# Kernel tuning notes

Measured on AMD Instinct MI355X. Metric: run time of the kernel, lower is better.

Reference implementation:

```python
import jax, jax.numpy as jnp
import numpy as np

TOP_K = 2
CAP_FACTOR = 1.25
AUX_COEF = 0.01
Z_COEF = 0.001


def setup_inputs() -> dict:
    key = jax.random.key(0)
    k1, k2 = jax.random.split(key)
    hidden_states = jax.random.normal(k1, (4, 1024, 4096), dtype=jnp.float32)
    # gate_proj weight, torch Linear layout [out=E, in=H]
    W = jax.random.normal(k2, (8, 4096), dtype=jnp.float32) * 0.02
    return {"hidden_states": hidden_states, "W": W}


def reference(hidden_states, W):
    B, S, H = hidden_states.shape
    E = W.shape[0]
    T = B * S
    K = TOP_K
    C = max(int(T * K / E * CAP_FACTOR), 1)  # expert capacity

    x = hidden_states.reshape(T, H)
    gate_logits = x @ W.T                           # [T, E]
    top_v, top_i = jax.lax.top_k(gate_logits, K)    # [T, K]
    top_w = jax.nn.softmax(top_v, axis=-1)          # [T, K]

    # Flatten assignments in (token-major, k-minor) order, matching the
    # sequential python loop. Slot within an expert = number of prior
    # assignments to that expert (exclusive prefix count).
    e = top_i.reshape(-1)                           # [T*K]
    oh = jax.nn.one_hot(e, E, dtype=jnp.int32)      # [T*K, E]
    pos = jnp.sum(jnp.cumsum(oh, axis=0) * oh, axis=-1) - 1  # [T*K]
    valid = pos < C
    pos_c = jnp.minimum(pos, C - 1)
    tok = jnp.arange(T * K) // K
    w = top_w.reshape(-1)

    combine_weights = jnp.zeros((T, E, C), dtype=hidden_states.dtype)
    combine_weights = combine_weights.at[tok, e, pos_c].add(jnp.where(valid, w, 0.0))
    dispatch_mask = jnp.zeros((T, E, C), dtype=jnp.int32)
    dispatch_mask = dispatch_mask.at[tok, e, pos_c].add(valid.astype(jnp.int32)).astype(bool)

    # aux losses (module is in training mode by default)
    gate_probs = jax.nn.softmax(gate_logits, axis=-1)
    mean_gate_prob = gate_probs.mean(axis=0)                      # [E]
    tokens_per_expert = dispatch_mask.sum(axis=(0, 2)).astype(jnp.float32)
    tokens_per_expert = tokens_per_expert / tokens_per_expert.sum()
    load_balancing_loss = AUX_COEF * E * jnp.sum(mean_gate_prob * tokens_per_expert)
    router_z_loss = Z_COEF * jnp.mean(jax.nn.logsumexp(gate_logits, axis=-1))

    return dispatch_mask, combine_weights, top_i, load_balancing_loss, router_z_loss
```

## Files before the change

kernel.cpp:

```cpp
#include <hip/hip_runtime.h>
#include <math.h>

#define TT   4096
#define HH   4096
#define EE   8
#define KTOP 2
#define CAP  1280
#define TEC  ((size_t)TT * EE * CAP)

#define GATE_BLOCKS 256
#define ZERO_BLOCKS 4096

typedef __attribute__((ext_vector_type(4))) float f32x4;


__global__ __launch_bounds__(256) void fused_kernel(
    const float* __restrict__ x, const float* __restrict__ W,
    float* __restrict__ out, float* __restrict__ ws_part,
    int* __restrict__ ws_e, float* __restrict__ ws_w)
{
    int tid = threadIdx.x;

    if (blockIdx.x >= GATE_BLOCKS) {
        size_t zb = blockIdx.x - GATE_BLOCKS;
        f32x4* p = (f32x4*)out;
        const size_t per = (2 * TEC / 4) / ZERO_BLOCKS;
        size_t base = zb * per;
        f32x4 z = {0.f, 0.f, 0.f, 0.f};
#pragma unroll 4
        for (size_t i = tid; i < per; i += 256)
            __builtin_nontemporal_store(z, &p[base + i]);
        return;
    }

    __shared__ float bacc[9];
    if (tid < 9) bacc[tid] = 0.f;
    __syncthreads();

    int wave = tid >> 6;
    int lane = tid & 63;
    int t0 = (blockIdx.x * 4 + wave) * 4;

    const float4* __restrict__ W4 = (const float4*)W;
    const float4* __restrict__ X4 = (const float4*)x;

    float acc[4][8];
#pragma unroll
    for (int tt = 0; tt < 4; ++tt)
#pragma unroll
        for (int e = 0; e < 8; ++e) acc[tt][e] = 0.f;

    for (int jj = 0; jj < 16; ++jj) {
        int ci = jj * 64 + lane;
        float4 wv[8];
#pragma unroll
        for (int e = 0; e < 8; ++e) wv[e] = W4[e * 1024 + ci];
#pragma unroll
        for (int tt = 0; tt < 4; ++tt) {
            float4 xv = X4[(size_t)(t0 + tt) * 1024 + ci];
#pragma unroll
            for (int e = 0; e < 8; ++e) {
                acc[tt][e] = fmaf(xv.x, wv[e].x, acc[tt][e]);
                acc[tt][e] = fmaf(xv.y, wv[e].y, acc[tt][e]);
                acc[tt][e] = fmaf(xv.z, wv[e].z, acc[tt][e]);
                acc[tt][e] = fmaf(xv.w, wv[e].w, acc[tt][e]);
            }
        }
    }

#pragma unroll
    for (int tt = 0; tt < 4; ++tt)
#pragma unroll
        for (int e = 0; e < 8; ++e) {
#pragma unroll
            for (int s = 32; s >= 1; s >>= 1)
                acc[tt][e] += __shfl_xor(acc[tt][e], s, 64);
        }

    if (lane == 0) {
        for (int tt = 0; tt < 4; ++tt) {
            int t = t0 + tt;
            float l[8];
#pragma unroll
            for (int e = 0; e < 8; ++e) l[e] = acc[tt][e];

            float m = l[0];
#pragma unroll
            for (int e = 1; e < 8; ++e) m = fmaxf(m, l[e]);
            float p[8], s = 0.f;
#pragma unroll
            for (int e = 0; e < 8; ++e) { p[e] = expf(l[e] - m); s += p[e]; }
            float inv = 1.f / s;
#pragma unroll
            for (int e = 0; e < 8; ++e) atomicAdd(&bacc[e], p[e] * inv);
            atomicAdd(&bacc[8], m + logf(s));

            int i0 = 0;
#pragma unroll
            for (int e = 1; e < 8; ++e) if (l[e] > l[i0]) i0 = e;
            int i1 = (i0 == 0) ? 1 : 0;
#pragma unroll
            for (int e = 0; e < 8; ++e) if (e != i0 && l[e] > l[i1]) i1 = e;

            float w0 = 1.f / (1.f + expf(l[i1] - l[i0]));
            float w1 = 1.f - w0;

            float* out_topi = out + 2 * TEC;
            out_topi[t * 2 + 0] = (float)i0;
            out_topi[t * 2 + 1] = (float)i1;
            ws_e[t * 2 + 0] = i0;
            ws_e[t * 2 + 1] = i1;
            ws_w[t * 2 + 0] = w0;
            ws_w[t * 2 + 1] = w1;
        }
    }
    __syncthreads();
    if (tid < 9) ws_part[blockIdx.x * 9 + tid] = bacc[tid];
}

__global__ __launch_bounds__(256) void assign_kernel(
    const int* __restrict__ ws_e, const float* __restrict__ ws_w,
    const float* __restrict__ ws_part, float* __restrict__ out)
{
    __shared__ int   scnt[256][8];
    __shared__ int   ssum[8][8];
    __shared__ int   stot[8];
    __shared__ float lacc[9];

    int tid = threadIdx.x;
    if (tid < 9) lacc[tid] = 0.f;
    __syncthreads();

#pragma unroll
    for (int j = 0; j < 9; ++j)
        atomicAdd(&lacc[j], ws_part[tid * 9 + j]);

    const int PER = (TT * KTOP) / 256;
    int i0 = tid * PER;
    int cnt[8];
#pragma unroll
    for (int e = 0; e < 8; ++e) cnt[e] = 0;
    for (int j = 0; j < PER; ++j) cnt[ws_e[i0 + j]]++;
#pragma unroll
    for (int e = 0; e < 8; ++e) scnt[tid][e] = cnt[e];
    __syncthreads();

    if (tid < 64) {
        int e = tid & 7, seg = tid >> 3;
        int run = 0;
        for (int j = seg * 32; j < seg * 32 + 32; ++j) {
            int v = scnt[j][e];
            scnt[j][e] = run;
            run += v;
        }
        ssum[seg][e] = run;
    }
    __syncthreads();
    if (tid < 8) {
        int run = 0;
        for (int s = 0; s < 8; ++s) {
            int v = ssum[s][tid];
            ssum[s][tid] = run;
            run += v;
        }
        stot[tid] = run;
    }
    __syncthreads();

    int seg = tid >> 5;
    int base[8];
#pragma unroll
    for (int e = 0; e < 8; ++e) base[e] = scnt[tid][e] + ssum[seg][e];

    for (int j = 0; j < PER; ++j) {
        int i = i0 + j;
        int e = ws_e[i];
        int pos = base[e]++;
        if (pos < CAP) {
            int tok = i >> 1;
            size_t idx = (size_t)tok * (EE * CAP) + (size_t)e * CAP + pos;
            out[idx] = 1.0f;
            out[TEC + idx] = ws_w[i];
        }
    }
    __syncthreads();

    if (tid == 0) {
        int tot_valid = 0;
        int ve[8];
#pragma unroll
        for (int e = 0; e < 8; ++e) { ve[e] = min(stot[e], CAP); tot_valid += ve[e]; }
        float lbl = 0.f;
#pragma unroll
        for (int e = 0; e < 8; ++e)
            lbl += (lacc[e] / (float)TT) * ((float)ve[e] / (float)tot_valid);
        lbl *= 0.01f * (float)EE;
        float zl = 0.001f * lacc[8] / (float)TT;
        out[2 * TEC + TT * KTOP + 0] = lbl;
        out[2 * TEC + TT * KTOP + 1] = zl;
    }
}

extern "C" void kernel_launch(void* const* d_in, const int* in_sizes, int n_in,
                              void* d_out, int out_size, void* d_ws, size_t ws_size,
                              hipStream_t stream) {
    const float* x = (const float*)d_in[0];
    const float* W = (const float*)d_in[1];
    float* out = (float*)d_out;

    float* ws_part = (float*)d_ws;
    int*   ws_e    = (int*)((char*)d_ws + GATE_BLOCKS * 9 * 4);
    float* ws_w    = (float*)((char*)d_ws + GATE_BLOCKS * 9 * 4 + (size_t)TT * KTOP * 4);

    fused_kernel<<<GATE_BLOCKS + ZERO_BLOCKS, 256, 0, stream>>>(
        x, W, out, ws_part, ws_e, ws_w);

    assign_kernel<<<1, 256, 0, stream>>>(ws_e, ws_w, ws_part, out);
}
```

Before: 108.8 us.

## Split gate, scan, and zero-plus-scatter into three kernels with wider gate grid

The gate GEMV now uses 1024 blocks, with four waves splitting the hidden dimension of each 4-token group and combining partial sums through shared memory. Per-token softmax stats are written to the workspace and summed in the scan kernel. The scan kernel now only computes slot positions, and a new kernel zeroes each 2-token slab of the two big outputs and then scatters that slab's entries, removing the serial single-block scatter. The cost is an extra launch, the zero fill no longer overlapping the gate work, and regular stores replacing the nontemporal ones.

Result: slower. 113.1 us (+3.9%).

```diff
diff --git a/kernel.cpp b/kernel.cpp
--- a/kernel.cpp
+++ b/kernel.cpp
@@ -8,41 +8,26 @@
 #define CAP  1280
 #define TEC  ((size_t)TT * EE * CAP)
 
-#define GATE_BLOCKS 256
-#define ZERO_BLOCKS 4096
+#define GATE_BLOCKS 1024
+#define ZS_BLOCKS   4096
 
 typedef __attribute__((ext_vector_type(4))) float f32x4;
 
 
-__global__ __launch_bounds__(256) void fused_kernel(
+__global__ __launch_bounds__(256) void gate_kernel(
     const float* __restrict__ x, const float* __restrict__ W,
     float* __restrict__ out, float* __restrict__ ws_part,
     int* __restrict__ ws_e, float* __restrict__ ws_w)
 {
-    int tid = threadIdx.x;
-
-    if (blockIdx.x >= GATE_BLOCKS) {
-        size_t zb = blockIdx.x - GATE_BLOCKS;
-        f32x4* p = (f32x4*)out;
-        const size_t per = (2 * TEC / 4) / ZERO_BLOCKS;
-        size_t base = zb * per;
-        f32x4 z = {0.f, 0.f, 0.f, 0.f};
-#pragma unroll 4
-        for (size_t i = tid; i < per; i += 256)
-            __builtin_nontemporal_store(z, &p[base + i]);
-        return;
-    }
-
-    __shared__ float bacc[9];
-    if (tid < 9) bacc[tid] = 0.f;
-    __syncthreads();
-
+    __shared__ float wpart[4][4][8];
+
+    int tid  = threadIdx.x;
     int wave = tid >> 6;
     int lane = tid & 63;
-    int t0 = (blockIdx.x * 4 + wave) * 4;
-
+    int t0   = blockIdx.x * 4;
+
+    const float4* __restrict__ X4 = (const float4*)x;
     const float4* __restrict__ W4 = (const float4*)W;
-    const float4* __restrict__ X4 = (const float4*)x;
 
     float acc[4][8];
 #pragma unroll
@@ -50,8 +35,9 @@
 #pragma unroll
         for (int e = 0; e < 8; ++e) acc[tt][e] = 0.f;
 
-    for (int jj = 0; jj < 16; ++jj) {
-        int ci = jj * 64 + lane;
+#pragma unroll
+    for (int j = 0; j < 4; ++j) {
+        int ci = wave * 256 + j * 64 + lane;
         float4 wv[8];
 #pragma unroll
         for (int e = 0; e < 8; ++e) wv[e] = W4[e * 1024 + ci];
@@ -78,49 +64,55 @@
         }
 
     if (lane == 0) {
-        for (int tt = 0; tt < 4; ++tt) {
-            int t = t0 + tt;
-            float l[8];
-#pragma unroll
-            for (int e = 0; e < 8; ++e) l[e] = acc[tt][e];
-
-            float m = l[0];
-#pragma unroll
-            for (int e = 1; e < 8; ++e) m = fmaxf(m, l[e]);
-            float p[8], s = 0.f;
-#pragma unroll
-            for (int e = 0; e < 8; ++e) { p[e] = expf(l[e] - m); s += p[e]; }
-            float inv = 1.f / s;
-#pragma unroll
-            for (int e = 0; e < 8; ++e) atomicAdd(&bacc[e], p[e] * inv);
-            atomicAdd(&bacc[8], m + logf(s));
-
-            int i0 = 0;
-#pragma unroll
-            for (int e = 1; e < 8; ++e) if (l[e] > l[i0]) i0 = e;
-            int i1 = (i0 == 0) ? 1 : 0;
-#pragma unroll
-            for (int e = 0; e < 8; ++e) if (e != i0 && l[e] > l[i1]) i1 = e;
-
-            float w0 = 1.f / (1.f + expf(l[i1] - l[i0]));
-            float w1 = 1.f - w0;
-
-            float* out_topi = out + 2 * TEC;
-            out_topi[t * 2 + 0] = (float)i0;
-            out_topi[t * 2 + 1] = (float)i1;
-            ws_e[t * 2 + 0] = i0;
-            ws_e[t * 2 + 1] = i1;
-            ws_w[t * 2 + 0] = w0;
-            ws_w[t * 2 + 1] = w1;
-        }
-    }
-    __syncthreads();
-    if (tid < 9) ws_part[blockIdx.x * 9 + tid] = bacc[tid];
-}
-
-__global__ __launch_bounds__(256) void assign_kernel(
-    const int* __restrict__ ws_e, const float* __restrict__ ws_w,
-    const float* __restrict__ ws_part, float* __restrict__ out)
+#pragma unroll
+        for (int tt = 0; tt < 4; ++tt)
+#pragma unroll
+            for (int e = 0; e < 8; ++e) wpart[wave][tt][e] = acc[tt][e];
+    }
+    __syncthreads();
+
+    if (tid < 4) {
+        int t = t0 + tid;
+        float l[8];
+#pragma unroll
+        for (int e = 0; e < 8; ++e)
+            l[e] = wpart[0][tid][e] + wpart[1][tid][e] +
+                   wpart[2][tid][e] + wpart[3][tid][e];
+
+        float m = l[0];
+#pragma unroll
+        for (int e = 1; e < 8; ++e) m = fmaxf(m, l[e]);
+        float p[8], s = 0.f;
+#pragma unroll
+        for (int e = 0; e < 8; ++e) { p[e] = expf(l[e] - m); s += p[e]; }
+        float inv = 1.f / s;
+#pragma unroll
+        for (int e = 0; e < 8; ++e) ws_part[t * 9 + e] = p[e] * inv;
+        ws_part[t * 9 + 8] = m + logf(s);
+
+        int i0 = 0;
+#pragma unroll
+        for (int e = 1; e < 8; ++e) if (l[e] > l[i0]) i0 = e;
+        int i1 = (i0 == 0) ? 1 : 0;
+#pragma unroll
+        for (int e = 0; e < 8; ++e) if (e != i0 && l[e] > l[i1]) i1 = e;
+
+        float w0 = 1.f / (1.f + expf(l[i1] - l[i0]));
+        float w1 = 1.f - w0;
+
+        float* out_topi = out + 2 * TEC;
+        out_topi[t * 2 + 0] = (float)i0;
+        out_topi[t * 2 + 1] = (float)i1;
+        ws_e[t * 2 + 0] = i0;
+        ws_e[t * 2 + 1] = i1;
+        ws_w[t * 2 + 0] = w0;
+        ws_w[t * 2 + 1] = w1;
+    }
+}
+
+__global__ __launch_bounds__(256) void scan_kernel(
+    const int* __restrict__ ws_e, const float* __restrict__ ws_part,
+    int* __restrict__ ws_pos, float* __restrict__ out)
 {
     __shared__ int   scnt[256][8];
     __shared__ int   ssum[8][8];
@@ -131,9 +123,18 @@
     if (tid < 9) lacc[tid] = 0.f;
     __syncthreads();
 
-#pragma unroll
-    for (int j = 0; j < 9; ++j)
-        atomicAdd(&lacc[j], ws_part[tid * 9 + j]);
+    {
+        float r[9];
+#pragma unroll
+        for (int j = 0; j < 9; ++j) r[j] = 0.f;
+        for (int k = 0; k < TT / 256; ++k) {
+            const float* q = ws_part + (size_t)(tid * (TT / 256) + k) * 9;
+#pragma unroll
+            for (int j = 0; j < 9; ++j) r[j] += q[j];
+        }
+#pragma unroll
+        for (int j = 0; j < 9; ++j) atomicAdd(&lacc[j], r[j]);
+    }
 
     const int PER = (TT * KTOP) / 256;
     int i0 = tid * PER;
@@ -167,23 +168,18 @@
     }
     __syncthreads();
 
-    int seg = tid >> 5;
-    int base[8];
-#pragma unroll
-    for (int e = 0; e < 8; ++e) base[e] = scnt[tid][e] + ssum[seg][e];
-
-    for (int j = 0; j < PER; ++j) {
-        int i = i0 + j;
-        int e = ws_e[i];
-        int pos = base[e]++;
-        if (pos < CAP) {
-            int tok = i >> 1;
-            size_t idx = (size_t)tok * (EE * CAP) + (size_t)e * CAP + pos;
-            out[idx] = 1.0f;
-            out[TEC + idx] = ws_w[i];
-        }
-    }
-    __syncthreads();
+    {
+        int seg = tid >> 5;
+        int base[8];
+#pragma unroll
+        for (int e = 0; e < 8; ++e) base[e] = scnt[tid][e] + ssum[seg][e];
+        for (int j = 0; j < PER; ++j) {
+            int i = i0 + j;
+            int e = ws_e[i];
+            int pos = base[e]++;
+            ws_pos[i] = (pos < CAP) ? pos : -1;
+        }
+    }
 
     if (tid == 0) {
         int tot_valid = 0;
@@ -201,6 +197,37 @@
     }
 }
 
+__global__ __launch_bounds__(256) void zs_kernel(
+    const int* __restrict__ ws_e, const int* __restrict__ ws_pos,
+    const float* __restrict__ ws_w, float* __restrict__ out)
+{
+    int tid = threadIdx.x;
+    int b   = blockIdx.x;
+
+    const int per4 = (int)((2 * TEC / 4) / ZS_BLOCKS);
+    f32x4* p = (f32x4*)out + (size_t)b * per4;
+    f32x4 z = {0.f, 0.f, 0.f, 0.f};
+#pragma unroll 4
+    for (int i = tid; i < per4; i += 256)
+        p[i] = z;
+
+    __syncthreads();
+
+    if (tid < 4) {
+        bool is_mask = (b < ZS_BLOCKS / 2);
+        int tbase = is_mask ? 2 * b : 2 * (b - ZS_BLOCKS / 2);
+        int lt = tid >> 1, k = tid & 1;
+        int i = (tbase + lt) * 2 + k;
+        int pos = ws_pos[i];
+        if (pos >= 0) {
+            int e = ws_e[i];
+            float v = is_mask ? 1.0f : ws_w[i];
+            float* fp = out + (size_t)b * (per4 * 4);
+            fp[lt * (EE * CAP) + e * CAP + pos] = v;
+        }
+    }
+}
+
 extern "C" void kernel_launch(void* const* d_in, const int* in_sizes, int n_in,
                               void* d_out, int out_size, void* d_ws, size_t ws_size,
                               hipStream_t stream) {
@@ -208,12 +235,13 @@
     const float* W = (const float*)d_in[1];
     float* out = (float*)d_out;
 
-    float* ws_part = (float*)d_ws;
-    int*   ws_e    = (int*)((char*)d_ws + GATE_BLOCKS * 9 * 4);
-    float* ws_w    = (float*)((char*)d_ws + GATE_BLOCKS * 9 * 4 + (size_t)TT * KTOP * 4);
-
-    fused_kernel<<<GATE_BLOCKS + ZERO_BLOCKS, 256, 0, stream>>>(
-        x, W, out, ws_part, ws_e, ws_w);
-
-    assign_kernel<<<1, 256, 0, stream>>>(ws_e, ws_w, ws_part, out);
-}
+    char* ws = (char*)d_ws;
+    float* ws_part = (float*)ws;
+    int*   ws_e    = (int*)(ws + (size_t)TT * 9 * 4);
+    float* ws_w    = (float*)(ws + (size_t)TT * 9 * 4 + (size_t)TT * KTOP * 4);
+    int*   ws_pos  = (int*)(ws + (size_t)TT * 9 * 4 + (size_t)TT * KTOP * 8);
+
+    gate_kernel<<<GATE_BLOCKS, 256, 0, stream>>>(x, W, out, ws_part, ws_e, ws_w);
+    scan_kernel<<<1, 256, 0, stream>>>(ws_e, ws_part, ws_pos, out);
+    zs_kernel<<<ZS_BLOCKS, 256, 0, stream>>>(ws_e, ws_pos, ws_w, out);
+}
```
